# Performance work log

Hardware: AMD Instinct MI355X
Metric: run time of the kernel (lower is better)

The kernel has to match this reference:

```python
import jax, jax.numpy as jnp
import numpy as np

N, E = 100000, 1600000
NFEAT, NHID, NOUT, NHEADS = 512, 64, 64, 8
ALPHA = 0.2  # LeakyReLU negative slope


def setup_inputs() -> dict:
    key = jax.random.key(0)
    ks = jax.random.split(key, 12)
    feat = jax.random.normal(ks[0], (N, NFEAT), dtype=jnp.float32)
    edge_index = jax.random.randint(ks[1], (2, E), 0, N, dtype=jnp.int32)
    s = 0.05
    return {
        "feat": feat,
        "edge_index": edge_index,
        "fW_w": jax.random.normal(ks[2], (NHEADS, NHID, NFEAT), dtype=jnp.float32) * s,
        "fW_b": jnp.zeros((NHEADS, NHID), dtype=jnp.float32),
        "a_src": jax.random.normal(ks[3], (NHEADS, NHID), dtype=jnp.float32) * s,
        "a_dest": jax.random.normal(ks[4], (NHEADS, NHID), dtype=jnp.float32) * s,
        "W0": jax.random.normal(ks[5], (NHEADS, NHID, NFEAT), dtype=jnp.float32) * s,
        "b0": jnp.zeros((NHEADS, NHID), dtype=jnp.float32),
        "W1": jax.random.normal(ks[6], (NHEADS, NHID, NHEADS * NHID), dtype=jnp.float32) * s,
        "b1": jnp.zeros((NHEADS, NHID), dtype=jnp.float32),
        "lin_w": jax.random.normal(ks[7], (NOUT, NHEADS * NHID), dtype=jnp.float32) * s,
        "lin_b": jnp.zeros((NOUT,), dtype=jnp.float32),
    }


def reference(feat, edge_index, fW_w, fW_b, a_src, a_dest, W0, b0, W1, b1, lin_w, lin_b):
    n = feat.shape[0]
    row, col = edge_index[0], edge_index[1]

    # feature attention (all heads at once): h = fW(feat)  [N,H,D]
    h = jnp.einsum('nf,hdf->nhd', feat, fW_w) + fW_b
    f1 = jnp.einsum('nhd,hd->nh', h, a_src)   # [N,H]
    f2 = jnp.einsum('nhd,hd->nh', h, a_dest)  # [N,H]
    e = f1[row] + f2[col]                     # [E,H]
    e = jnp.where(e > 0, e, ALPHA * e)        # LeakyReLU
    # sparse softmax over each row's neighborhood (dim=1 of adj)
    m = jax.ops.segment_max(e, row, num_segments=n)    # [N,H]
    ex = jnp.exp(e - m[row])
    denom = jax.ops.segment_sum(ex, row, num_segments=n)
    attn = ex / denom[row]                    # [E,H]

    def spmm(vals, xw):  # vals [E], xw [N,D] -> [N,D]
        return jax.ops.segment_sum(vals[:, None] * xw[col], row, num_segments=n)

    x = feat
    for Wl, bl in ((W0, b0), (W1, b1)):
        outs = []
        for hidx in range(NHEADS):
            xw = x @ Wl[hidx].T + bl[hidx]           # [N,NHID]
            outs.append(jax.nn.elu(spmm(attn[:, hidx], xw)))
        x = jnp.concatenate(outs, axis=1)            # [N, H*NHID]

    return x @ lin_w.T + lin_b
```

## Files before the change

kernel.cpp:

```cpp
#include <hip/hip_runtime.h>
#include <hip/hip_bf16.h>
#include <math.h>

#define NFEAT 512
#define NHID  64
#define NHEADS 8
#define HD    512
#define NOUT  64

typedef _Float16 half8 __attribute__((ext_vector_type(8)));
typedef _Float16 half4 __attribute__((ext_vector_type(4)));
typedef float floatx4 __attribute__((ext_vector_type(4)));

__global__ void g_k(const float* __restrict__ fW_w, const float* __restrict__ fW_b,
                    const float* __restrict__ a_src, const float* __restrict__ a_dest,
                    float* __restrict__ G, float* __restrict__ C16)
{
    int idx = blockIdx.x * blockDim.x + threadIdx.x;
    if (idx < 16 * 512) {
        int r = idx >> 9;
        int f = idx & 511;
        int h = r & 7;
        const float* a = (r < 8) ? a_src : a_dest;
        float s = 0.f;
        #pragma unroll 8
        for (int d = 0; d < 64; ++d)
            s = fmaf(fW_w[(size_t)(h * 64 + d) * 512 + f], a[h * 64 + d], s);
        G[(size_t)r * 512 + f] = s;
    } else if (idx < 16 * 512 + 16) {
        int r = idx - 16 * 512;
        int h = r & 7;
        const float* a = (r < 8) ? a_src : a_dest;
        float s = 0.f;
        for (int d = 0; d < 64; ++d)
            s = fmaf(fW_b[h * 64 + d], a[h * 64 + d], s);
        C16[r] = s;
    }
}

#define FB_BM 128
#define FB_BK 64
__global__ __launch_bounds__(256) void f1f2_k(const float* __restrict__ feat,
    const float* __restrict__ G, const float* __restrict__ C16,
    float* __restrict__ f1, float* __restrict__ f2,
    _Float16* __restrict__ featH, int M)
{
    __shared__ float As[FB_BK][FB_BM + 4];
    __shared__ float Gs[16][FB_BK + 1];
    int tid = threadIdx.x;
    int tx = tid & 15;
    int ty = tid >> 4;
    int m0 = blockIdx.x * FB_BM;
    float acc[8] = {0.f, 0.f, 0.f, 0.f, 0.f, 0.f, 0.f, 0.f};

    for (int k0 = 0; k0 < NFEAT; k0 += FB_BK) {
        __syncthreads();
        #pragma unroll
        for (int j = 0; j < 8; ++j) {
            int fid = tid + 256 * j;
            int ml = fid >> 4;
            int k4 = fid & 15;
            float4 v = make_float4(0.f, 0.f, 0.f, 0.f);
            int gm = m0 + ml;
            if (gm < M) {
                v = *(const float4*)(feat + (size_t)gm * NFEAT + k0 + k4 * 4);
                half4 hv;
                hv[0] = (_Float16)v.x; hv[1] = (_Float16)v.y;
                hv[2] = (_Float16)v.z; hv[3] = (_Float16)v.w;
                *(half4*)(featH + (size_t)gm * NFEAT + k0 + k4 * 4) = hv;
            }
            As[k4 * 4 + 0][ml] = v.x;
            As[k4 * 4 + 1][ml] = v.y;
            As[k4 * 4 + 2][ml] = v.z;
            As[k4 * 4 + 3][ml] = v.w;
        }
        {
            int gr = tid >> 4;
            int k4 = tid & 15;
            float4 v = *(const float4*)(G + (size_t)gr * 512 + k0 + k4 * 4);
            Gs[gr][k4 * 4 + 0] = v.x;
            Gs[gr][k4 * 4 + 1] = v.y;
            Gs[gr][k4 * 4 + 2] = v.z;
            Gs[gr][k4 * 4 + 3] = v.w;
        }
        __syncthreads();
        #pragma unroll 16
        for (int kk = 0; kk < FB_BK; ++kk) {
            float g = Gs[tx][kk];
            #pragma unroll
            for (int i = 0; i < 8; ++i)
                acc[i] = fmaf(As[kk][ty + 16 * i], g, acc[i]);
        }
    }
    float c = C16[tx];
    #pragma unroll
    for (int i = 0; i < 8; ++i) {
        int gm = m0 + ty + 16 * i;
        if (gm < M) {
            float v = acc[i] + c;
            if (tx < 8) f1[(size_t)gm * 8 + tx] = v;
            else        f2[(size_t)gm * 8 + (tx - 8)] = v;
        }
    }
}

__global__ void zero_k(int* __restrict__ deg, int* __restrict__ fill, int n)
{
    int i = blockIdx.x * blockDim.x + threadIdx.x;
    if (i < n) { deg[i] = 0; fill[i] = 0; }
}

__global__ void count_k(const int* __restrict__ ei, int* __restrict__ deg, int E)
{
    int e = blockIdx.x * blockDim.x + threadIdx.x;
    if (e < E) atomicAdd(&deg[ei[e]], 1);
}

__global__ __launch_bounds__(1024) void bscan_k(const int* __restrict__ deg,
    int* __restrict__ row_ptr, int* __restrict__ bsum, int n)
{
    __shared__ int sh[1024];
    int tid = threadIdx.x;
    int i = blockIdx.x * 1024 + tid;
    int x = (i < n) ? deg[i] : 0;
    sh[tid] = x;
    __syncthreads();
    for (int off = 1; off < 1024; off <<= 1) {
        int v = (tid >= off) ? sh[tid - off] : 0;
        __syncthreads();
        sh[tid] += v;
        __syncthreads();
    }
    if (i < n) row_ptr[i] = sh[tid] - x;
    if (tid == 1023) bsum[blockIdx.x] = sh[1023];
}

__global__ void sscan_k(int* __restrict__ bsum, int nb)
{
    if (blockIdx.x == 0 && threadIdx.x == 0) {
        int run = 0;
        for (int b = 0; b < nb; ++b) { int t = bsum[b]; bsum[b] = run; run += t; }
    }
}

__global__ void addoff_k(int* __restrict__ row_ptr, const int* __restrict__ bsum,
                         int n, int Etot)
{
    int i = blockIdx.x * blockDim.x + threadIdx.x;
    if (i < n) row_ptr[i] += bsum[i >> 10];
    if (i == 0) row_ptr[n] = Etot;
}

__global__ void fill_k(const int* __restrict__ ei, const int* __restrict__ row_ptr,
                       int* __restrict__ fill, int* __restrict__ col_s, int E)
{
    int e = blockIdx.x * blockDim.x + threadIdx.x;
    if (e >= E) return;
    int r = ei[e];
    int c = ei[E + e];
    int o = atomicAdd(&fill[r], 1);
    col_s[row_ptr[r] + o] = c;
}

__global__ void attn_k(const int* __restrict__ row_ptr, const int* __restrict__ col_s,
                       const float* __restrict__ f1, const float* __restrict__ f2,
                       float* __restrict__ attn_s, float* __restrict__ inv_den,
                       int n_rows)
{
    int idx = blockIdx.x * blockDim.x + threadIdx.x;
    int n = idx >> 3;
    int h = idx & 7;
    if (n >= n_rows) return;
    int s = row_ptr[n], e = row_ptr[n + 1];
    float F1 = f1[(size_t)n * 8 + h];
    float den = 0.f;
    for (int p = s; p < e; ++p) {
        int c = col_s[p];
        float t = F1 + f2[(size_t)c * 8 + h];
        t = (t > 0.f) ? t : 0.2f * t;
        float ex = expf(t);
        den += ex;
        __builtin_nontemporal_store(ex, attn_s + (size_t)p * 8 + h);
    }
    inv_den[(size_t)n * 8 + h] = (den > 0.f) ? 1.f / den : 0.f;
}

__global__ void cvt_f16_k(const float* __restrict__ in, _Float16* __restrict__ out,
                          size_t n)
{
    size_t i = ((size_t)blockIdx.x * blockDim.x + threadIdx.x) * 8;
    if (i >= n) return;
    float4 a = *(const float4*)(in + i);
    float4 b = *(const float4*)(in + i + 4);
    half8 h;
    h[0] = (_Float16)a.x; h[1] = (_Float16)a.y; h[2] = (_Float16)a.z; h[3] = (_Float16)a.w;
    h[4] = (_Float16)b.x; h[5] = (_Float16)b.y; h[6] = (_Float16)b.z; h[7] = (_Float16)b.w;
    *(half8*)(out + i) = h;
}

#define TM 128
#define TN 128
#define TK 64
__global__ __launch_bounds__(256) void gemm_f16_mfma(
    const _Float16* __restrict__ A,
    const _Float16* __restrict__ B,
    const float* __restrict__ bias,
    _Float16* __restrict__ C,
    int M, int N, int K)
{
    __shared__ _Float16 smem_h[TM * TK + TN * TK];
    _Float16* Ash = smem_h;
    _Float16* Bsh = smem_h + TM * TK;
    int tid = threadIdx.x;
    int wave = tid >> 6;
    int lane = tid & 63;
    int m0 = blockIdx.y * TM;
    int n0 = blockIdx.x * TN;
    int wm = (wave & 1) * 64;
    int wn = (wave >> 1) * 64;

    floatx4 acc[4][4] = {};

    int fm = lane & 15;
    int q  = lane >> 4;
    int lrow = lane >> 3;
    int lcol = (lane & 7) ^ lrow;

    for (int k0 = 0; k0 < K; k0 += TK) {
        __syncthreads();
        #pragma unroll
        for (int t = 0; t < 4; ++t) {
            int r = wave * 8 + t * 32;
            int gr = m0 + r + lrow;
            if (gr > M - 1) gr = M - 1;
            const _Float16* ga = A + (size_t)gr * K + k0 + lcol * 8;
            __builtin_amdgcn_global_load_lds(
                (const __attribute__((address_space(1))) void*)ga,
                (__attribute__((address_space(3))) void*)&Ash[r * TK], 16, 0, 0);
            const _Float16* gb = B + (size_t)(n0 + r + lrow) * K + k0 + lcol * 8;
            __builtin_amdgcn_global_load_lds(
                (const __attribute__((address_space(1))) void*)gb,
                (__attribute__((address_space(3))) void*)&Bsh[r * TK], 16, 0, 0);
        }
        __syncthreads();
        #pragma unroll
        for (int kq = 0; kq < 2; ++kq) {
            half8 af[4], bf[4];
            int sw = ((kq << 2) + q);
            #pragma unroll
            for (int i = 0; i < 4; ++i) {
                int ar = wm + i * 16 + fm;
                af[i] = *(const half8*)&Ash[ar * TK + ((sw ^ (fm & 7)) << 3)];
                int br = wn + i * 16 + fm;
                bf[i] = *(const half8*)&Bsh[br * TK + ((sw ^ (fm & 7)) << 3)];
            }
            #pragma unroll
            for (int i = 0; i < 4; ++i)
                #pragma unroll
                for (int j = 0; j < 4; ++j)
                    acc[i][j] = __builtin_amdgcn_mfma_f32_16x16x32_f16(af[i], bf[j], acc[i][j], 0, 0, 0);
        }
    }
    int cn = lane & 15;
    int rq = lane >> 4;
    _Float16* Csh = smem_h + wave * 1024;
    #pragma unroll
    for (int i = 0; i < 4; ++i) {
        __syncthreads();
        #pragma unroll
        for (int j = 0; j < 4; ++j) {
            int col = j * 16 + cn;
            float bsv = bias[n0 + wn + col];
            int scol = col ^ (rq * 16);
            #pragma unroll
            for (int r = 0; r < 4; ++r) {
                int row = rq * 4 + r;
                Csh[row * 64 + scol] = (_Float16)(acc[i][j][r] + bsv);
            }
        }
        __syncthreads();
        #pragma unroll
        for (int t = 0; t < 2; ++t) {
            int row = t * 8 + (lane >> 3);
            int c0 = (lane & 7) * 8;
            int sc0 = c0 ^ (((row >> 2) & 3) * 16);
            half8 v = *(const half8*)&Csh[row * 64 + sc0];
            int gm = m0 + wm + i * 16 + row;
            if (gm < M)
                *(half8*)&C[(size_t)gm * N + n0 + wn + c0] = v;
        }
    }
}

#define FG_TM 256
#define FG_TK 32
__global__ __launch_bounds__(256) void gemm_f16_n64(
    const _Float16* __restrict__ A,
    const _Float16* __restrict__ B,
    const float* __restrict__ bias,
    float* __restrict__ C,
    int M, int K)
{
    __shared__ _Float16 Ash[FG_TM * FG_TK];
    __shared__ _Float16 Bsh[64 * FG_TK];
    int tid = threadIdx.x;
    int wave = tid >> 6;
    int lane = tid & 63;
    int m0 = blockIdx.x * FG_TM;
    int wm = wave * 64;

    floatx4 acc[4][4] = {};
    int fm = lane & 15;
    int q  = lane >> 4;

    for (int k0 = 0; k0 < K; k0 += FG_TK) {
        __syncthreads();
        #pragma unroll
        for (int t = 0; t < 4; ++t) {
            int r = wave * 16 + t * 64;
            int gr = m0 + r + (lane >> 2);
            if (gr > M - 1) gr = M - 1;
            const _Float16* ga = A + (size_t)gr * K + k0 + (lane & 3) * 8;
            __builtin_amdgcn_global_load_lds(
                (const __attribute__((address_space(1))) void*)ga,
                (__attribute__((address_space(3))) void*)&Ash[r * FG_TK], 16, 0, 0);
        }
        {
            int r = wave * 16;
            const _Float16* gb = B + (size_t)(r + (lane >> 2)) * K + k0 + (lane & 3) * 8;
            __builtin_amdgcn_global_load_lds(
                (const __attribute__((address_space(1))) void*)gb,
                (__attribute__((address_space(3))) void*)&Bsh[r * FG_TK], 16, 0, 0);
        }
        __syncthreads();
        half8 af[4], bf[4];
        #pragma unroll
        for (int i = 0; i < 4; ++i) {
            af[i] = *(const half8*)&Ash[(wm + i * 16 + fm) * FG_TK + q * 8];
            bf[i] = *(const half8*)&Bsh[(i * 16 + fm) * FG_TK + q * 8];
        }
        #pragma unroll
        for (int i = 0; i < 4; ++i)
            #pragma unroll
            for (int j = 0; j < 4; ++j)
                acc[i][j] = __builtin_amdgcn_mfma_f32_16x16x32_f16(af[i], bf[j], acc[i][j], 0, 0, 0);
    }
    int cn = lane & 15;
    int rq = lane >> 4;
    #pragma unroll
    for (int i = 0; i < 4; ++i) {
        #pragma unroll
        for (int j = 0; j < 4; ++j) {
            int gn = j * 16 + cn;
            float bsv = bias[gn];
            #pragma unroll
            for (int r = 0; r < 4; ++r) {
                int gm = m0 + wm + i * 16 + rq * 4 + r;
                if (gm < M)
                    C[(size_t)gm * NOUT + gn] = acc[i][j][r] + bsv;
            }
        }
    }
}

__global__ __launch_bounds__(256) void agg_h_k(const int* __restrict__ row_ptr,
    const int* __restrict__ col_s, const float* __restrict__ attn_s,
    const float* __restrict__ inv_den, const _Float16* __restrict__ xw,
    _Float16* __restrict__ out, int n_rows)
{
    int wid = (blockIdx.x * blockDim.x + threadIdx.x) >> 6;
    int lane = threadIdx.x & 63;
    if (wid >= n_rows) return;
    int s = row_ptr[wid], e = row_ptr[wid + 1];
    int h = lane >> 3;
    float acc0[8] = {0.f, 0.f, 0.f, 0.f, 0.f, 0.f, 0.f, 0.f};
    float acc1[8] = {0.f, 0.f, 0.f, 0.f, 0.f, 0.f, 0.f, 0.f};
    float acc2[8] = {0.f, 0.f, 0.f, 0.f, 0.f, 0.f, 0.f, 0.f};
    float acc3[8] = {0.f, 0.f, 0.f, 0.f, 0.f, 0.f, 0.f, 0.f};
    int p = s;
    for (; p + 4 <= e; p += 4) {
        int c0 = col_s[p];
        int c1 = col_s[p + 1];
        int c2 = col_s[p + 2];
        int c3 = col_s[p + 3];
        float a0 = attn_s[(size_t)p * 8 + h];
        float a1 = attn_s[(size_t)(p + 1) * 8 + h];
        float a2 = attn_s[(size_t)(p + 2) * 8 + h];
        float a3 = attn_s[(size_t)(p + 3) * 8 + h];
        half8 x0 = *(const half8*)(xw + (size_t)c0 * HD + lane * 8);
        half8 x1 = *(const half8*)(xw + (size_t)c1 * HD + lane * 8);
        half8 x2 = *(const half8*)(xw + (size_t)c2 * HD + lane * 8);
        half8 x3 = *(const half8*)(xw + (size_t)c3 * HD + lane * 8);
        #pragma unroll
        for (int u = 0; u < 8; ++u) {
            acc0[u] = fmaf(a0, (float)x0[u], acc0[u]);
            acc1[u] = fmaf(a1, (float)x1[u], acc1[u]);
            acc2[u] = fmaf(a2, (float)x2[u], acc2[u]);
            acc3[u] = fmaf(a3, (float)x3[u], acc3[u]);
        }
    }
    for (; p < e; ++p) {
        int c0 = col_s[p];
        float a0 = attn_s[(size_t)p * 8 + h];
        half8 x0 = *(const half8*)(xw + (size_t)c0 * HD + lane * 8);
        #pragma unroll
        for (int u = 0; u < 8; ++u)
            acc0[u] = fmaf(a0, (float)x0[u], acc0[u]);
    }
    float inv = inv_den[(size_t)wid * 8 + h];
    half8 o;
    #pragma unroll
    for (int u = 0; u < 8; ++u) {
        float v = ((acc0[u] + acc1[u]) + (acc2[u] + acc3[u])) * inv;
        v = (v > 0.f) ? v : (expf(v) - 1.f);
        o[u] = (_Float16)v;
    }
    __builtin_nontemporal_store(o, (half8*)(out + (size_t)wid * HD + lane * 8));
}

extern "C" void kernel_launch(void* const* d_in, const int* in_sizes, int n_in,
                              void* d_out, int out_size, void* d_ws, size_t ws_size,
                              hipStream_t stream)
{
    const float* feat   = (const float*)d_in[0];
    const int*   ei     = (const int*)  d_in[1];
    const float* fW_w   = (const float*)d_in[2];
    const float* fW_b   = (const float*)d_in[3];
    const float* a_src  = (const float*)d_in[4];
    const float* a_dest = (const float*)d_in[5];
    const float* W0     = (const float*)d_in[6];
    const float* b0     = (const float*)d_in[7];
    const float* W1     = (const float*)d_in[8];
    const float* b1     = (const float*)d_in[9];
    const float* lin_w  = (const float*)d_in[10];
    const float* lin_b  = (const float*)d_in[11];
    float* outp = (float*)d_out;

    const int N = in_sizes[0] / NFEAT;
    const int E = in_sizes[1] / 2;
    const int NB = (N + 1023) / 1024;

    char* ws = (char*)d_ws;
    size_t off = 0;
    auto carve = [&](size_t bytes) -> char* {
        char* p = ws + off;
        off += (bytes + 255) & ~(size_t)255;
        return p;
    };
    float*     G       = (float*)carve(16 * 512 * sizeof(float));
    float*     C16     = (float*)carve(16 * sizeof(float));
    float*     f1      = (float*)carve((size_t)N * 8 * sizeof(float));
    float*     f2      = (float*)carve((size_t)N * 8 * sizeof(float));
    int*       deg     = (int*)  carve((size_t)N * sizeof(int));
    int*       fillc   = (int*)  carve((size_t)N * sizeof(int));
    int*       row_ptr = (int*)  carve(((size_t)N + 1) * sizeof(int));
    int*       bsum    = (int*)  carve((size_t)NB * sizeof(int));
    int*       col_s   = (int*)  carve((size_t)E * sizeof(int));
    float*     attn_s  = (float*)carve((size_t)E * 8 * sizeof(float));
    float*     inv_den = (float*)carve((size_t)N * 8 * sizeof(float));
    _Float16*  W0h     = (_Float16*)carve((size_t)HD * NFEAT * sizeof(_Float16));
    _Float16*  W1h     = (_Float16*)carve((size_t)HD * HD * sizeof(_Float16));
    _Float16*  linWh   = (_Float16*)carve((size_t)NOUT * HD * sizeof(_Float16));
    _Float16*  hbuf1   = (_Float16*)carve((size_t)N * NFEAT * sizeof(_Float16));
    _Float16*  xwH     = (_Float16*)carve((size_t)N * HD * sizeof(_Float16));
    (void)ws_size; (void)n_in; (void)out_size;

    g_k<<<(16 * 512 + 16 + 255) / 256, 256, 0, stream>>>(fW_w, fW_b, a_src, a_dest, G, C16);
    f1f2_k<<<(N + FB_BM - 1) / FB_BM, 256, 0, stream>>>(feat, G, C16, f1, f2, hbuf1, N);
    zero_k<<<(N + 255) / 256, 256, 0, stream>>>(deg, fillc, N);
    count_k<<<(E + 255) / 256, 256, 0, stream>>>(ei, deg, E);
    bscan_k<<<NB, 1024, 0, stream>>>(deg, row_ptr, bsum, N);
    sscan_k<<<1, 64, 0, stream>>>(bsum, NB);
    addoff_k<<<(N + 255) / 256, 256, 0, stream>>>(row_ptr, bsum, N, E);
    fill_k<<<(E + 255) / 256, 256, 0, stream>>>(ei, row_ptr, fillc, col_s, E);
    attn_k<<<((size_t)N * 8 + 255) / 256, 256, 0, stream>>>(row_ptr, col_s, f1, f2, attn_s, inv_den, N);

    cvt_f16_k<<<(int)(((size_t)HD * NFEAT / 8 + 255) / 256), 256, 0, stream>>>(W0, W0h, (size_t)HD * NFEAT);
    cvt_f16_k<<<(int)(((size_t)HD * HD / 8 + 255) / 256), 256, 0, stream>>>(W1, W1h, (size_t)HD * HD);
    cvt_f16_k<<<(int)(((size_t)NOUT * HD / 8 + 255) / 256), 256, 0, stream>>>(lin_w, linWh, (size_t)NOUT * HD);

    gemm_f16_mfma<<<dim3(HD / TN, (N + TM - 1) / TM), 256, 0, stream>>>(
        hbuf1, W0h, b0, xwH, N, HD, NFEAT);
    agg_h_k<<<((size_t)N * 64 + 255) / 256, 256, 0, stream>>>(
        row_ptr, col_s, attn_s, inv_den, xwH, hbuf1, N);
    gemm_f16_mfma<<<dim3(HD / TN, (N + TM - 1) / TM), 256, 0, stream>>>(
        hbuf1, W1h, b1, xwH, N, HD, HD);
    agg_h_k<<<((size_t)N * 64 + 255) / 256, 256, 0, stream>>>(
        row_ptr, col_s, attn_s, inv_den, xwH, hbuf1, N);
    gemm_f16_n64<<<(N + FG_TM - 1) / FG_TM, 256, 0, stream>>>(
        hbuf1, linWh, lin_b, outp, N, HD);
}
```

Measured before the change: 1.307 ms.

## Store xw and attention head-major and aggregate each head separately

After: 1.725 ms. 1.32x slower.

```diff
diff --git a/kernel.cpp b/kernel.cpp
--- a/kernel.cpp
+++ b/kernel.cpp
@@ -164,8 +164,8 @@
 
 __global__ void attn_k(const int* __restrict__ row_ptr, const int* __restrict__ col_s,
                        const float* __restrict__ f1, const float* __restrict__ f2,
-                       float* __restrict__ attn_s, float* __restrict__ inv_den,
-                       int n_rows)
+                       float* __restrict__ attn_t, float* __restrict__ inv_t,
+                       int n_rows, int E)
 {
     int idx = blockIdx.x * blockDim.x + threadIdx.x;
     int n = idx >> 3;
@@ -173,6 +173,7 @@
     if (n >= n_rows) return;
     int s = row_ptr[n], e = row_ptr[n + 1];
     float F1 = f1[(size_t)n * 8 + h];
+    float* at = attn_t + (size_t)h * E;
     float den = 0.f;
     for (int p = s; p < e; ++p) {
         int c = col_s[p];
@@ -180,9 +181,9 @@
         t = (t > 0.f) ? t : 0.2f * t;
         float ex = expf(t);
         den += ex;
-        __builtin_nontemporal_store(ex, attn_s + (size_t)p * 8 + h);
-    }
-    inv_den[(size_t)n * 8 + h] = (den > 0.f) ? 1.f / den : 0.f;
+        at[p] = ex;
+    }
+    inv_t[(size_t)h * n_rows + n] = (den > 0.f) ? 1.f / den : 0.f;
 }
 
 __global__ void cvt_f16_k(const float* __restrict__ in, _Float16* __restrict__ out,
@@ -263,6 +264,7 @@
     }
     int cn = lane & 15;
     int rq = lane >> 4;
+    int head = (n0 + wn) >> 6;
     _Float16* Csh = smem_h + wave * 1024;
     #pragma unroll
     for (int i = 0; i < 4; ++i) {
@@ -287,7 +289,7 @@
             half8 v = *(const half8*)&Csh[row * 64 + sc0];
             int gm = m0 + wm + i * 16 + row;
             if (gm < M)
-                *(half8*)&C[(size_t)gm * N + n0 + wn + c0] = v;
+                *(half8*)&C[((size_t)head * M + gm) * 64 + c0] = v;
         }
     }
 }
@@ -364,58 +366,51 @@
 }
 
 __global__ __launch_bounds__(256) void agg_h_k(const int* __restrict__ row_ptr,
-    const int* __restrict__ col_s, const float* __restrict__ attn_s,
-    const float* __restrict__ inv_den, const _Float16* __restrict__ xw,
-    _Float16* __restrict__ out, int n_rows)
-{
-    int wid = (blockIdx.x * blockDim.x + threadIdx.x) >> 6;
-    int lane = threadIdx.x & 63;
+    const int* __restrict__ col_s, const float* __restrict__ attn_t,
+    const float* __restrict__ inv_t, const _Float16* __restrict__ xw,
+    _Float16* __restrict__ out, int n_rows, int E)
+{
+    int head  = blockIdx.x & 7;
+    int rowblk = blockIdx.x >> 3;
+    int wave  = threadIdx.x >> 6;
+    int lane  = threadIdx.x & 63;
+    int wid   = rowblk * 4 + wave;
     if (wid >= n_rows) return;
     int s = row_ptr[wid], e = row_ptr[wid + 1];
-    int h = lane >> 3;
-    float acc0[8] = {0.f, 0.f, 0.f, 0.f, 0.f, 0.f, 0.f, 0.f};
-    float acc1[8] = {0.f, 0.f, 0.f, 0.f, 0.f, 0.f, 0.f, 0.f};
-    float acc2[8] = {0.f, 0.f, 0.f, 0.f, 0.f, 0.f, 0.f, 0.f};
-    float acc3[8] = {0.f, 0.f, 0.f, 0.f, 0.f, 0.f, 0.f, 0.f};
-    int p = s;
-    for (; p + 4 <= e; p += 4) {
-        int c0 = col_s[p];
-        int c1 = col_s[p + 1];
-        int c2 = col_s[p + 2];
-        int c3 = col_s[p + 3];
-        float a0 = attn_s[(size_t)p * 8 + h];
-        float a1 = attn_s[(size_t)(p + 1) * 8 + h];
-        float a2 = attn_s[(size_t)(p + 2) * 8 + h];
-        float a3 = attn_s[(size_t)(p + 3) * 8 + h];
-        half8 x0 = *(const half8*)(xw + (size_t)c0 * HD + lane * 8);
-        half8 x1 = *(const half8*)(xw + (size_t)c1 * HD + lane * 8);
-        half8 x2 = *(const half8*)(xw + (size_t)c2 * HD + lane * 8);
-        half8 x3 = *(const half8*)(xw + (size_t)c3 * HD + lane * 8);
-        #pragma unroll
-        for (int u = 0; u < 8; ++u) {
-            acc0[u] = fmaf(a0, (float)x0[u], acc0[u]);
-            acc1[u] = fmaf(a1, (float)x1[u], acc1[u]);
-            acc2[u] = fmaf(a2, (float)x2[u], acc2[u]);
-            acc3[u] = fmaf(a3, (float)x3[u], acc3[u]);
-        }
-    }
-    for (; p < e; ++p) {
-        int c0 = col_s[p];
-        float a0 = attn_s[(size_t)p * 8 + h];
-        half8 x0 = *(const half8*)(xw + (size_t)c0 * HD + lane * 8);
+    int eg = lane >> 3;
+    int cs = lane & 7;
+    const float*    attn_h = attn_t + (size_t)head * E;
+    const _Float16* xw_h   = xw + (size_t)head * n_rows * 64;
+
+    float acc[8] = {0.f, 0.f, 0.f, 0.f, 0.f, 0.f, 0.f, 0.f};
+    for (int p = s; p < e; p += 8) {
+        int pe = p + eg;
+        bool act = pe < e;
+        int pc = act ? pe : s;
+        int c  = col_s[pc];
+        float a = act ? attn_h[pe] : 0.f;
+        half8 x = *(const half8*)(xw_h + (size_t)c * 64 + cs * 8);
         #pragma unroll
         for (int u = 0; u < 8; ++u)
-            acc0[u] = fmaf(a0, (float)x0[u], acc0[u]);
-    }
-    float inv = inv_den[(size_t)wid * 8 + h];
+            acc[u] = fmaf(a, (float)x[u], acc[u]);
+    }
+    #pragma unroll
+    for (int m = 8; m <= 32; m <<= 1) {
+        #pragma unroll
+        for (int u = 0; u < 8; ++u)
+            acc[u] += __shfl_xor(acc[u], m);
+    }
+    float inv = inv_t[(size_t)head * n_rows + wid];
     half8 o;
     #pragma unroll
     for (int u = 0; u < 8; ++u) {
-        float v = ((acc0[u] + acc1[u]) + (acc2[u] + acc3[u])) * inv;
+        float v = acc[u] * inv;
         v = (v > 0.f) ? v : (expf(v) - 1.f);
         o[u] = (_Float16)v;
     }
-    __builtin_nontemporal_store(o, (half8*)(out + (size_t)wid * HD + lane * 8));
+    if (lane < 8)
+        __builtin_nontemporal_store(o,
+            (half8*)(out + (size_t)wid * HD + head * 64 + lane * 8));
 }
 
 extern "C" void kernel_launch(void* const* d_in, const int* in_sizes, int n_in,
@@ -456,8 +451,8 @@
     int*       row_ptr = (int*)  carve(((size_t)N + 1) * sizeof(int));
     int*       bsum    = (int*)  carve((size_t)NB * sizeof(int));
     int*       col_s   = (int*)  carve((size_t)E * sizeof(int));
-    float*     attn_s  = (float*)carve((size_t)E * 8 * sizeof(float));
-    float*     inv_den = (float*)carve((size_t)N * 8 * sizeof(float));
+    float*     attn_t  = (float*)carve((size_t)E * 8 * sizeof(float));
+    float*     inv_t   = (float*)carve((size_t)N * 8 * sizeof(float));
     _Float16*  W0h     = (_Float16*)carve((size_t)HD * NFEAT * sizeof(_Float16));
     _Float16*  W1h     = (_Float16*)carve((size_t)HD * HD * sizeof(_Float16));
     _Float16*  linWh   = (_Float16*)carve((size_t)NOUT * HD * sizeof(_Float16));
@@ -473,20 +468,22 @@
     sscan_k<<<1, 64, 0, stream>>>(bsum, NB);
     addoff_k<<<(N + 255) / 256, 256, 0, stream>>>(row_ptr, bsum, N, E);
     fill_k<<<(E + 255) / 256, 256, 0, stream>>>(ei, row_ptr, fillc, col_s, E);
-    attn_k<<<((size_t)N * 8 + 255) / 256, 256, 0, stream>>>(row_ptr, col_s, f1, f2, attn_s, inv_den, N);
+    attn_k<<<((size_t)N * 8 + 255) / 256, 256, 0, stream>>>(row_ptr, col_s, f1, f2, attn_t, inv_t, N, E);
 
     cvt_f16_k<<<(int)(((size_t)HD * NFEAT / 8 + 255) / 256), 256, 0, stream>>>(W0, W0h, (size_t)HD * NFEAT);
     cvt_f16_k<<<(int)(((size_t)HD * HD / 8 + 255) / 256), 256, 0, stream>>>(W1, W1h, (size_t)HD * HD);
     cvt_f16_k<<<(int)(((size_t)NOUT * HD / 8 + 255) / 256), 256, 0, stream>>>(lin_w, linWh, (size_t)NOUT * HD);
 
+    const int agg_blocks = 8 * ((N + 3) / 4);
+
     gemm_f16_mfma<<<dim3(HD / TN, (N + TM - 1) / TM), 256, 0, stream>>>(
         hbuf1, W0h, b0, xwH, N, HD, NFEAT);
-    agg_h_k<<<((size_t)N * 64 + 255) / 256, 256, 0, stream>>>(
-        row_ptr, col_s, attn_s, inv_den, xwH, hbuf1, N);
+    agg_h_k<<<agg_blocks, 256, 0, stream>>>(
+        row_ptr, col_s, attn_t, inv_t, xwH, hbuf1, N, E);
     gemm_f16_mfma<<<dim3(HD / TN, (N + TM - 1) / TM), 256, 0, stream>>>(
         hbuf1, W1h, b1, xwH, N, HD, HD);
-    agg_h_k<<<((size_t)N * 64 + 255) / 256, 256, 0, stream>>>(
-        row_ptr, col_s, attn_s, inv_den, xwH, hbuf1, N);
+    agg_h_k<<<agg_blocks, 256, 0, stream>>>(
+        row_ptr, col_s, attn_t, inv_t, xwH, hbuf1, N, E);
     gemm_f16_n64<<<(N + FG_TM - 1) / FG_TM, 256, 0, stream>>>(
         hbuf1, linWh, lin_b, outp, N, HD);
 }
```
